# Performance work log

Measured on AMD Instinct MI355X. Metric: run time of the kernel, lower is better.

## Reference

```python
import jax, jax.numpy as jnp
import numpy as np


def setup_inputs() -> dict:
    key = jax.random.key(0)
    k1, k2, k3 = jax.random.split(key, 3)
    in_features, out_features = 256, 256
    x = jax.random.normal(k1, (16, 128, in_features), dtype=jnp.float32)
    # weight[:, :, 0] = output mixing weights, weight[:, :, 1] = frequency weights
    weight = jax.random.normal(k2, (in_features, out_features, 2), dtype=jnp.float32) / np.sqrt(in_features)
    # bias[0] = output bias, bias[1:] = per-(in,out) phase
    bias = jax.random.normal(k3, (in_features + 1, out_features), dtype=jnp.float32) / np.sqrt(in_features)
    return {"x": x, "weight": weight, "bias": bias}


def reference(x, weight, bias):
    out_features = weight.shape[1]
    out_shape = x.shape[:-1] + (out_features,)
    xf = x.reshape(-1, x.shape[-1])  # [B, I]
    w_amp = weight[:, :, 0]   # [I, O]
    w_freq = weight[:, :, 1]  # [I, O]
    # bio = sin(x_bi * w_io + phase_io); out_bo = sum_i amp_io * bio
    bio = jnp.sin(jnp.einsum('bi,io->bio', xf, w_freq) + bias[1:, :])
    out = jnp.einsum('io,bio->bo', w_amp, bio) + bias[0, :]
    return out.reshape(out_shape)
```

## Files before the change

### kernel.cpp

```cpp
#include <hip/hip_runtime.h>


constexpr int IN_F   = 256;
constexpr int OUT_F  = 256;
constexpr int BROWS  = 2048;
constexpr int BTILE  = 8;
constexpr int ISPLIT = 16;
constexpr int ICHUNK = IN_F / ISPLIT;
constexpr int OPAIRS = 32;
constexpr int OSPLIT = 4;

#define INV2PI 0.15915494309189535f

__global__ __launch_bounds__(OPAIRS * ISPLIT, 8) void ripple_kernel(
    const float* __restrict__ x,
    const float* __restrict__ weight,
    const float* __restrict__ bias,
    float* __restrict__ out)
{
    const int tx = threadIdx.x;
    const int g  = threadIdx.y;
    const int ob = blockIdx.x & (OSPLIT - 1);
    const int bb = blockIdx.x >> 2;
    const int b0 = bb * BTILE;
    const int oc = ob * OPAIRS + tx;

    __shared__ __align__(16) float xs_t[IN_F * BTILE];
    __shared__ float2 red[ISPLIT / 2 - 1][BTILE][OPAIRS];

    {
        const int t  = g * OPAIRS + tx;
        const int r  = t & 7;
        const int i4 = t >> 3;
        const float4 v = ((const float4*)x)[(b0 + r) * (IN_F / 4) + i4];
        xs_t[(4 * i4 + 0) * BTILE + r] = v.x * INV2PI;
        xs_t[(4 * i4 + 1) * BTILE + r] = v.y * INV2PI;
        xs_t[(4 * i4 + 2) * BTILE + r] = v.z * INV2PI;
        xs_t[(4 * i4 + 3) * BTILE + r] = v.w * INV2PI;
    }
    __syncthreads();

    float acc0[BTILE], acc1[BTILE];
#pragma unroll
    for (int r = 0; r < BTILE; ++r) { acc0[r] = 0.0f; acc1[r] = 0.0f; }

    const float4* __restrict__ wq  = (const float4*)weight;
    const float2* __restrict__ ph2 = (const float2*)bias;

    const int i0 = g * ICHUNK;
#pragma unroll 2
    for (int ii = 0; ii < ICHUNK; ++ii) {
        const int i = i0 + ii;
        const float4 w = wq[i * (OUT_F / 2) + oc];
        const float2 p = ph2[(i + 1) * (OUT_F / 2) + oc];
        const float px = p.x * INV2PI;
        const float py = p.y * INV2PI;
        const float4 xa = *(const float4*)&xs_t[i * BTILE];
        const float4 xb = *(const float4*)&xs_t[i * BTILE + 4];
        const float xv[BTILE] = {xa.x, xa.y, xa.z, xa.w, xb.x, xb.y, xb.z, xb.w};
#pragma unroll
        for (int r = 0; r < BTILE; ++r) {
            acc0[r] += w.x * __builtin_amdgcn_sinf(fmaf(xv[r], w.y, px));
            acc1[r] += w.z * __builtin_amdgcn_sinf(fmaf(xv[r], w.w, py));
        }
    }

#pragma unroll
    for (int r = 0; r < BTILE; ++r) {
        acc0[r] += __shfl_down(acc0[r], 32);
        acc1[r] += __shfl_down(acc1[r], 32);
    }

    const int wv = g >> 1;
    if ((g & 1) == 0 && wv > 0) {
#pragma unroll
        for (int r = 0; r < BTILE; ++r) red[wv - 1][r][tx] = make_float2(acc0[r], acc1[r]);
    }
    __syncthreads();
    if (g == 0) {
        const float2 bo = ph2[oc];
#pragma unroll
        for (int r = 0; r < BTILE; ++r) {
            float s0 = acc0[r], s1 = acc1[r];
#pragma unroll
            for (int k = 0; k < ISPLIT / 2 - 1; ++k) {
                const float2 t = red[k][r][tx];
                s0 += t.x; s1 += t.y;
            }
            ((float2*)out)[(b0 + r) * (OUT_F / 2) + oc] = make_float2(s0 + bo.x, s1 + bo.y);
        }
    }
}

extern "C" void kernel_launch(void* const* d_in, const int* in_sizes, int n_in,
                              void* d_out, int out_size, void* d_ws, size_t ws_size,
                              hipStream_t stream) {
    const float* x      = (const float*)d_in[0];
    const float* weight = (const float*)d_in[1];
    const float* bias   = (const float*)d_in[2];
    float* out          = (float*)d_out;

    dim3 grid((BROWS / BTILE) * OSPLIT);
    dim3 block(OPAIRS, ISPLIT);
    ripple_kernel<<<grid, block, 0, stream>>>(x, weight, bias, out);
}
```

Before: 76.97 us.

## Enlarge batch tile to 32 rows with 1024-thread blocks sharing weight loads

Each block now covers 32 batch rows, using 8 input-feature groups times 4 row subgroups (1024 threads). Each thread still handles 8 rows over 32 input features, so the weight and phase loads are amortized across more rows per block and fewer blocks are launched (256 instead of 1024). The cost is larger shared memory, a 1024-thread block that limits occupancy flexibility, and fewer blocks for load balancing across CUs.

```diff
diff --git a/kernel.cpp b/kernel.cpp
--- a/kernel.cpp
+++ b/kernel.cpp
@@ -4,90 +4,101 @@
 constexpr int IN_F   = 256;
 constexpr int OUT_F  = 256;
 constexpr int BROWS  = 2048;
-constexpr int BTILE  = 8;
-constexpr int ISPLIT = 16;
-constexpr int ICHUNK = IN_F / ISPLIT;
+constexpr int BTILE  = 32;
+constexpr int RSUB   = 4;
+constexpr int RPT    = 8;
+constexpr int IGRP   = 8;
+constexpr int ICHUNK = IN_F / IGRP;
 constexpr int OPAIRS = 32;
 constexpr int OSPLIT = 4;
 
 #define INV2PI 0.15915494309189535f
 
-__global__ __launch_bounds__(OPAIRS * ISPLIT, 8) void ripple_kernel(
+__global__ __launch_bounds__(1024) void ripple_kernel(
     const float* __restrict__ x,
     const float* __restrict__ weight,
     const float* __restrict__ bias,
     float* __restrict__ out)
 {
     const int tx = threadIdx.x;
-    const int g  = threadIdx.y;
+    const int y  = threadIdx.y;
+    const int ig = y & 7;
+    const int rs = y >> 3;
     const int ob = blockIdx.x & (OSPLIT - 1);
     const int bb = blockIdx.x >> 2;
     const int b0 = bb * BTILE;
     const int oc = ob * OPAIRS + tx;
 
+
     __shared__ __align__(16) float xs_t[IN_F * BTILE];
-    __shared__ float2 red[ISPLIT / 2 - 1][BTILE][OPAIRS];
+    __shared__ float2 red[3][RSUB][RPT][OPAIRS];
 
     {
-        const int t  = g * OPAIRS + tx;
-        const int r  = t & 7;
-        const int i4 = t >> 3;
-        const float4 v = ((const float4*)x)[(b0 + r) * (IN_F / 4) + i4];
-        xs_t[(4 * i4 + 0) * BTILE + r] = v.x * INV2PI;
-        xs_t[(4 * i4 + 1) * BTILE + r] = v.y * INV2PI;
-        xs_t[(4 * i4 + 2) * BTILE + r] = v.z * INV2PI;
-        xs_t[(4 * i4 + 3) * BTILE + r] = v.w * INV2PI;
+        const int t  = tx + 32 * y;
+        const int r  = t & 31;
+        const int c4 = t >> 5;
+#pragma unroll
+        for (int k = 0; k < 2; ++k) {
+            const int c = c4 + 32 * k;
+            const float4 v = ((const float4*)x)[(b0 + r) * (IN_F / 4) + c];
+            xs_t[(4 * c + 0) * BTILE + r] = v.x * INV2PI;
+            xs_t[(4 * c + 1) * BTILE + r] = v.y * INV2PI;
+            xs_t[(4 * c + 2) * BTILE + r] = v.z * INV2PI;
+            xs_t[(4 * c + 3) * BTILE + r] = v.w * INV2PI;
+        }
     }
     __syncthreads();
 
-    float acc0[BTILE], acc1[BTILE];
+    float2 acc[RPT];
 #pragma unroll
-    for (int r = 0; r < BTILE; ++r) { acc0[r] = 0.0f; acc1[r] = 0.0f; }
+    for (int r = 0; r < RPT; ++r) acc[r] = make_float2(0.0f, 0.0f);
 
     const float4* __restrict__ wq  = (const float4*)weight;
     const float2* __restrict__ ph2 = (const float2*)bias;
 
-    const int i0 = g * ICHUNK;
-#pragma unroll 2
+    const int i0 = ig * ICHUNK;
+    const int r0 = rs * RPT;
+#pragma unroll 4
     for (int ii = 0; ii < ICHUNK; ++ii) {
         const int i = i0 + ii;
         const float4 w = wq[i * (OUT_F / 2) + oc];
         const float2 p = ph2[(i + 1) * (OUT_F / 2) + oc];
         const float px = p.x * INV2PI;
         const float py = p.y * INV2PI;
-        const float4 xa = *(const float4*)&xs_t[i * BTILE];
-        const float4 xb = *(const float4*)&xs_t[i * BTILE + 4];
-        const float xv[BTILE] = {xa.x, xa.y, xa.z, xa.w, xb.x, xb.y, xb.z, xb.w};
+        const float4 xa = *(const float4*)&xs_t[i * BTILE + r0];
+        const float4 xb = *(const float4*)&xs_t[i * BTILE + r0 + 4];
+        const float xv[RPT] = {xa.x, xa.y, xa.z, xa.w, xb.x, xb.y, xb.z, xb.w};
 #pragma unroll
-        for (int r = 0; r < BTILE; ++r) {
-            acc0[r] += w.x * __builtin_amdgcn_sinf(fmaf(xv[r], w.y, px));
-            acc1[r] += w.z * __builtin_amdgcn_sinf(fmaf(xv[r], w.w, py));
+        for (int r = 0; r < RPT; ++r) {
+            acc[r].x += w.x * __builtin_amdgcn_sinf(fmaf(xv[r], w.y, px));
+            acc[r].y += w.z * __builtin_amdgcn_sinf(fmaf(xv[r], w.w, py));
         }
     }
 
 #pragma unroll
-    for (int r = 0; r < BTILE; ++r) {
-        acc0[r] += __shfl_down(acc0[r], 32);
-        acc1[r] += __shfl_down(acc1[r], 32);
+    for (int r = 0; r < RPT; ++r) {
+        acc[r].x += __shfl_down(acc[r].x, 32);
+        acc[r].y += __shfl_down(acc[r].y, 32);
     }
 
-    const int wv = g >> 1;
-    if ((g & 1) == 0 && wv > 0) {
+    const int pg = ig >> 1;
+    if ((ig & 1) == 0 && pg > 0) {
 #pragma unroll
-        for (int r = 0; r < BTILE; ++r) red[wv - 1][r][tx] = make_float2(acc0[r], acc1[r]);
+        for (int r = 0; r < RPT; ++r) red[pg - 1][rs][r][tx] = acc[r];
     }
     __syncthreads();
-    if (g == 0) {
+    if (ig == 0) {
         const float2 bo = ph2[oc];
 #pragma unroll
-        for (int r = 0; r < BTILE; ++r) {
-            float s0 = acc0[r], s1 = acc1[r];
+        for (int r = 0; r < RPT; ++r) {
+            float sx = acc[r].x, sy = acc[r].y;
 #pragma unroll
-            for (int k = 0; k < ISPLIT / 2 - 1; ++k) {
-                const float2 t = red[k][r][tx];
-                s0 += t.x; s1 += t.y;
+            for (int k = 0; k < 3; ++k) {
+                const float2 t = red[k][rs][r][tx];
+                sx += t.x; sy += t.y;
             }
-            ((float2*)out)[(b0 + r) * (OUT_F / 2) + oc] = make_float2(s0 + bo.x, s1 + bo.y);
+            ((float2*)out)[(b0 + r0 + r) * (OUT_F / 2) + oc] =
+                make_float2(sx + bo.x, sy + bo.y);
         }
     }
 }
@@ -101,6 +112,6 @@
     float* out          = (float*)d_out;
 
     dim3 grid((BROWS / BTILE) * OSPLIT);
-    dim3 block(OPAIRS, ISPLIT);
+    dim3 block(OPAIRS, BTILE);
     ripple_kernel<<<grid, block, 0, stream>>>(x, weight, bias, out);
 }
```

Result: no change. 75.67 us (-1.7%).
